# Performance work log

Measured on AMD Instinct MI355X. Metric: run time of the kernel, lower is better.

The kernel has to match this reference:

```python
import jax, jax.numpy as jnp
import numpy as np

EMBED_DIM = 256
NUM_WEIGHTS = 8
NUM_RELATIONS = 5
BATCH = 131072


def setup_inputs() -> dict:
    key = jax.random.key(0)
    k1, k2, k3, k4 = jax.random.split(key, 4)
    embeds1 = jax.random.normal(k1, (BATCH, EMBED_DIM), dtype=jnp.float32)
    embeds2 = jax.random.normal(k2, (BATCH, EMBED_DIM), dtype=jnp.float32)
    # Embedding(num_weights, D*D): torch default init is N(0,1)
    rel_embeds = jax.random.normal(k3, (NUM_WEIGHTS, EMBED_DIM * EMBED_DIM), dtype=jnp.float32)
    # weight_scalars ~ U(-stdv, stdv), stdv = 1/sqrt(num_relations)
    stdv = 1.0 / np.sqrt(NUM_RELATIONS)
    weight_scalars = jax.random.uniform(
        k4, (NUM_WEIGHTS, NUM_RELATIONS), dtype=jnp.float32, minval=-stdv, maxval=stdv
    )
    return {
        "embeds1": embeds1,
        "embeds2": embeds2,
        "rel_embeds": rel_embeds,
        "weight_scalars": weight_scalars,
    }


def reference(embeds1, embeds2, rel_embeds, weight_scalars):
    D = embeds1.shape[1]
    W = rel_embeds.shape[0]
    rel_mats = rel_embeds.reshape(W, D, D)  # [W, D, D]
    # Fused bilinear form u . R_w . v for every w: [B, W]
    basis_outputs = jnp.einsum("bi,wij,bj->bw", embeds1, rel_mats, embeds2)
    logit = basis_outputs @ weight_scalars  # [B, R]
    return logit
```

## Files before the change

kernel.cpp:

```cpp
#include <hip/hip_runtime.h>
#include <hip/hip_bf16.h>

#define ED   256
#define NW   8
#define NR   5
#define BM   64
#define BCOL 128
#define BK   64

typedef float  f32x4  __attribute__((ext_vector_type(4)));
typedef __bf16 bf16x8 __attribute__((ext_vector_type(8)));
typedef unsigned short u16;

__device__ __forceinline__ u16 f2bf(float f) {
    return __builtin_bit_cast(u16, __float2bfloat16(f));
}

__device__ __forceinline__ bf16x8 pack8(f32x4 a, f32x4 b) {
    union { u16 u[8]; bf16x8 v; } r;
    r.u[0] = f2bf(a[0]); r.u[1] = f2bf(a[1]); r.u[2] = f2bf(a[2]); r.u[3] = f2bf(a[3]);
    r.u[4] = f2bf(b[0]); r.u[5] = f2bf(b[1]); r.u[6] = f2bf(b[2]); r.u[7] = f2bf(b[3]);
    return r.v;
}

__global__ void prep_S(const float* __restrict__ rel,
                       const float* __restrict__ ws,
                       u16* __restrict__ S_T) {
    int idx = blockIdx.x * blockDim.x + threadIdx.x;
    if (idx >= ED * ED) return;
    int i = idx & (ED - 1);
    int j = idx >> 8;
    float acc[NR];
#pragma unroll
    for (int r = 0; r < NR; ++r) acc[r] = 0.f;
#pragma unroll
    for (int w = 0; w < NW; ++w) {
        float rv = rel[(size_t)w * ED * ED + (size_t)i * ED + j];
#pragma unroll
        for (int r = 0; r < NR; ++r) acc[r] += rv * ws[w * NR + r];
    }
#pragma unroll
    for (int r = 0; r < NR; ++r)
        S_T[((size_t)r * ED + j) * ED + i] = f2bf(acc[r]);
}

__global__ __launch_bounds__(256, 3) void bilinear_kernel(
    const float* __restrict__ e1, const float* __restrict__ e2,
    const u16* __restrict__ S_T, float* __restrict__ out) {

    __shared__ __align__(16) u16 Bbuf[2][BCOL * BK];
    __shared__ float Red[NR][BM][2];

    const int t    = threadIdx.x;
    const int wave = t >> 6;
    const int lane = t & 63;
    const int l15  = lane & 15;
    const int l4   = lane >> 4;
    const int wr   = wave >> 1;
    const int wc   = wave & 1;

    const int g       = blockIdx.x;
    const int per_xcd = gridDim.x >> 3;
    const int wgid    = (g & 7) * per_xcd + (g >> 3);
    const int ch      = wgid & 1;
    const long b0     = (long)(wgid >> 1) * BM;

    auto STAGE = [&](int rr, int kb, int b) {
        const u16* gb = S_T + ((size_t)rr * ED + ch * BCOL) * ED + kb * BK;
#pragma unroll
        for (int q = 0; q < 4; ++q) {
            int s  = q * 256 + t;
            int j  = s >> 3;
            int c  = s & 7;
            int cl = c ^ (j & 7);
            const u16* gp = gb + (size_t)j * ED + cl * 8;
            u16* lp = &Bbuf[b][(size_t)(q * 256 + wave * 64) * 8];
            __builtin_amdgcn_global_load_lds(
                (const __attribute__((address_space(1))) unsigned int*)gp,
                (__attribute__((address_space(3))) unsigned int*)lp, 16, 0, 0);
        }
    };

    STAGE(0, 0, 0);

    bf16x8 av[2][8];
#pragma unroll
    for (int m = 0; m < 2; ++m) {
        const float* rowp = e1 + (b0 + wr * 32 + m * 16 + l15) * ED + l4 * 8;
#pragma unroll
        for (int kb = 0; kb < 8; ++kb) {
            f32x4 a = *(const f32x4*)(rowp + kb * 32);
            f32x4 b = *(const f32x4*)(rowp + kb * 32 + 4);
            av[m][kb] = pack8(a, b);
        }
    }

    unsigned e2p[2][4][2];
#pragma unroll
    for (int m = 0; m < 2; ++m)
#pragma unroll
        for (int reg = 0; reg < 4; ++reg) {
            const float* erow =
                e2 + (b0 + wr * 32 + m * 16 + l4 * 4 + reg) * ED
                   + ch * BCOL + wc * 64 + l15;
#pragma unroll
            for (int h = 0; h < 2; ++h) {
                float a = __builtin_nontemporal_load(erow + (2 * h) * 16);
                float b = __builtin_nontemporal_load(erow + (2 * h + 1) * 16);
                e2p[m][reg][h] = (unsigned)f2bf(a) | ((unsigned)f2bf(b) << 16);
            }
        }

    __syncthreads();

    for (int r = 0; r < NR; ++r) {
        f32x4 acc[2][4];
#pragma unroll
        for (int m = 0; m < 2; ++m)
#pragma unroll
            for (int n = 0; n < 4; ++n)
                acc[m][n] = f32x4{0.f, 0.f, 0.f, 0.f};

#pragma unroll
        for (int kb = 0; kb < 4; ++kb) {
            const int s   = r * 4 + kb;
            const int cur = s & 1;

            if (s + 1 < NR * 4) {
                const int rn = (kb == 3) ? r + 1 : r;
                const int kn = (kb + 1) & 3;
                STAGE(rn, kn, cur ^ 1);
            }

#pragma unroll
            for (int h = 0; h < 2; ++h) {
                bf16x8 bv[4];
#pragma unroll
                for (int n = 0; n < 4; ++n) {
                    int j  = wc * 64 + n * 16 + l15;
                    int lb = j * (BK * 2) + h * 64 + l4 * 16;
                    int pb = lb ^ ((j & 7) << 4);
                    bv[n] = *(const bf16x8*)((const char*)Bbuf[cur] + pb);
                }
#pragma unroll
                for (int m = 0; m < 2; ++m)
#pragma unroll
                    for (int n = 0; n < 4; ++n)
                        acc[m][n] = __builtin_amdgcn_mfma_f32_16x16x32_bf16(
                            av[m][kb * 2 + h], bv[n], acc[m][n], 0, 0, 0);
            }

            __syncthreads();
        }

#pragma unroll
        for (int m = 0; m < 2; ++m)
#pragma unroll
            for (int reg = 0; reg < 4; ++reg) {
                const int row = wr * 32 + m * 16 + l4 * 4 + reg;
                float p = 0.f;
#pragma unroll
                for (int n = 0; n < 4; ++n) {
                    unsigned u = e2p[m][reg][n >> 1];
                    unsigned bits = (n & 1) ? (u & 0xffff0000u) : (u << 16);
                    p += acc[m][n][reg] * __builtin_bit_cast(float, bits);
                }
#pragma unroll
                for (int off = 1; off < 16; off <<= 1)
                    p += __shfl_xor(p, off);
                if (l15 == 0) Red[r][row][wc] = p;
            }
    }

    __syncthreads();
    for (int idx = t; idx < BM * NR; idx += 256) {
        int row = idx / NR;
        int r   = idx - row * NR;
        atomicAdd(&out[(b0 + row) * NR + r], Red[r][row][0] + Red[r][row][1]);
    }
}

extern "C" void kernel_launch(void* const* d_in, const int* in_sizes, int n_in,
                              void* d_out, int out_size, void* d_ws, size_t ws_size,
                              hipStream_t stream) {
    const float* e1  = (const float*)d_in[0];
    const float* e2  = (const float*)d_in[1];
    const float* rel = (const float*)d_in[2];
    const float* ws  = (const float*)d_in[3];
    float* out = (float*)d_out;
    u16* S_T = (u16*)d_ws;

    prep_S<<<(ED * ED + 255) / 256, 256, 0, stream>>>(rel, ws, S_T);

    hipMemsetAsync(out, 0, (size_t)out_size * sizeof(float), stream);

    int B = in_sizes[0] / ED;
    int grid = (B / BM) * 2;
    bilinear_kernel<<<grid, 256, 0, stream>>>(e1, e2, S_T, out);
}
```

Before: 244.0 us.

## Load S matrix fragments directly from global into registers, drop LDS staging

Replaces the double-buffered LDS staging of the combined relation matrix (global_load_lds plus swizzled LDS reads and per-step barriers) with direct per-lane global loads of bf16x8 fragments into two register buffers. The loads are software-pipelined against the MFMAs, and the relation loop is fully unrolled. This removes the LDS traffic and the __syncthreads between k-steps. In exchange each of the 4 waves now fetches its own B fragments from global/L2, so B data is no longer shared through LDS across the two row-waves, and latency hiding depends on a prefetch distance of one MFMA group.

```diff
diff --git a/kernel.cpp b/kernel.cpp
--- a/kernel.cpp
+++ b/kernel.cpp
@@ -6,7 +6,6 @@
 #define NR   5
 #define BM   64
 #define BCOL 128
-#define BK   64
 
 typedef float  f32x4  __attribute__((ext_vector_type(4)));
 typedef __bf16 bf16x8 __attribute__((ext_vector_type(8)));
@@ -48,7 +47,6 @@
     const float* __restrict__ e1, const float* __restrict__ e2,
     const u16* __restrict__ S_T, float* __restrict__ out) {
 
-    __shared__ __align__(16) u16 Bbuf[2][BCOL * BK];
     __shared__ float Red[NR][BM][2];
 
     const int t    = threadIdx.x;
@@ -65,23 +63,15 @@
     const int ch      = wgid & 1;
     const long b0     = (long)(wgid >> 1) * BM;
 
-    auto STAGE = [&](int rr, int kb, int b) {
-        const u16* gb = S_T + ((size_t)rr * ED + ch * BCOL) * ED + kb * BK;
+    const u16* const Sbase =
+        S_T + ((size_t)(ch * BCOL + wc * 64 + l15)) * ED + l4 * 8;
+
+    bf16x8 bv0[4], bv1[4];
 #pragma unroll
-        for (int q = 0; q < 4; ++q) {
-            int s  = q * 256 + t;
-            int j  = s >> 3;
-            int c  = s & 7;
-            int cl = c ^ (j & 7);
-            const u16* gp = gb + (size_t)j * ED + cl * 8;
-            u16* lp = &Bbuf[b][(size_t)(q * 256 + wave * 64) * 8];
-            __builtin_amdgcn_global_load_lds(
-                (const __attribute__((address_space(1))) unsigned int*)gp,
-                (__attribute__((address_space(3))) unsigned int*)lp, 16, 0, 0);
-        }
-    };
-
-    STAGE(0, 0, 0);
+    for (int n = 0; n < 4; ++n) {
+        bv0[n] = *(const bf16x8*)(Sbase + (size_t)n * 16 * ED);
+        bv1[n] = *(const bf16x8*)(Sbase + (size_t)n * 16 * ED + 32);
+    }
 
     bf16x8 av[2][8];
 #pragma unroll
@@ -111,9 +101,10 @@
             }
         }
 
-    __syncthreads();
+#pragma unroll
+    for (int r = 0; r < NR; ++r) {
+        const u16* const Sr = Sbase + (size_t)r * ED * ED;
 
-    for (int r = 0; r < NR; ++r) {
         f32x4 acc[2][4];
 #pragma unroll
         for (int m = 0; m < 2; ++m)
@@ -122,35 +113,36 @@
                 acc[m][n] = f32x4{0.f, 0.f, 0.f, 0.f};
 
 #pragma unroll
-        for (int kb = 0; kb < 4; ++kb) {
-            const int s   = r * 4 + kb;
-            const int cur = s & 1;
+        for (int kp = 0; kp < 4; ++kp) {
+            const int s = r * 8 + kp * 2;
 
-            if (s + 1 < NR * 4) {
-                const int rn = (kb == 3) ? r + 1 : r;
-                const int kn = (kb + 1) & 3;
-                STAGE(rn, kn, cur ^ 1);
+#pragma unroll
+            for (int m = 0; m < 2; ++m)
+#pragma unroll
+                for (int n = 0; n < 4; ++n)
+                    acc[m][n] = __builtin_amdgcn_mfma_f32_16x16x32_bf16(
+                        av[m][kp * 2], bv0[n], acc[m][n], 0, 0, 0);
+            if (s + 2 < NR * 8) {
+                const u16* p = (kp < 3) ? (Sr + (kp * 2 + 2) * 32)
+                                        : (Sr + ED * ED);
+#pragma unroll
+                for (int n = 0; n < 4; ++n)
+                    bv0[n] = *(const bf16x8*)(p + (size_t)n * 16 * ED);
             }
 
 #pragma unroll
-            for (int h = 0; h < 2; ++h) {
-                bf16x8 bv[4];
+            for (int m = 0; m < 2; ++m)
 #pragma unroll
-                for (int n = 0; n < 4; ++n) {
-                    int j  = wc * 64 + n * 16 + l15;
-                    int lb = j * (BK * 2) + h * 64 + l4 * 16;
-                    int pb = lb ^ ((j & 7) << 4);
-                    bv[n] = *(const bf16x8*)((const char*)Bbuf[cur] + pb);
-                }
+                for (int n = 0; n < 4; ++n)
+                    acc[m][n] = __builtin_amdgcn_mfma_f32_16x16x32_bf16(
+                        av[m][kp * 2 + 1], bv1[n], acc[m][n], 0, 0, 0);
+            if (s + 3 < NR * 8) {
+                const u16* p = (kp < 3) ? (Sr + (kp * 2 + 3) * 32)
+                                        : (Sr + ED * ED + 32);
 #pragma unroll
-                for (int m = 0; m < 2; ++m)
-#pragma unroll
-                    for (int n = 0; n < 4; ++n)
-                        acc[m][n] = __builtin_amdgcn_mfma_f32_16x16x32_bf16(
-                            av[m][kb * 2 + h], bv[n], acc[m][n], 0, 0, 0);
+                for (int n = 0; n < 4; ++n)
+                    bv1[n] = *(const bf16x8*)(p + (size_t)n * 16 * ED);
             }
-
-            __syncthreads();
         }
 
 #pragma unroll
```

After: 439.1 us. 80.0% more time.

## Make S slab LDS-resident and loop persistent workgroups over row passes

Applied to the files above, without the earlier changes.

Each 512-thread workgroup loads a fixed 64-column, 128-k slab of the combined relation matrices for all five relations into LDS once. It then loops over eight passes of 256 batch rows, which removes the per-step double-buffered S staging and its barriers. The grid becomes a fixed 512 blocks split four ways over output columns and two ways over k, so every block reads a different e1/e2 slice and writes partial sums to the output with atomics. The cost is many more global atomics, because there is no LDS reduction before the atomic step. The grid size is hardcoded for the batch of 131072, and there is no prefetch overlap between passes.

```diff
diff --git a/kernel.cpp b/kernel.cpp
--- a/kernel.cpp
+++ b/kernel.cpp
@@ -4,9 +4,10 @@
 #define ED   256
 #define NW   8
 #define NR   5
-#define BM   64
-#define BCOL 128
-#define BK   64
+#define CS   64
+#define KH   128
+#define NPASS 8
+#define RPP  256
 
 typedef float  f32x4  __attribute__((ext_vector_type(4)));
 typedef __bf16 bf16x8 __attribute__((ext_vector_type(8)));
@@ -44,139 +45,120 @@
         S_T[((size_t)r * ED + j) * ED + i] = f2bf(acc[r]);
 }
 
-__global__ __launch_bounds__(256, 3) void bilinear_kernel(
+__global__ __launch_bounds__(512, 4) void bilinear_kernel(
     const float* __restrict__ e1, const float* __restrict__ e2,
     const u16* __restrict__ S_T, float* __restrict__ out) {
 
-    __shared__ __align__(16) u16 Bbuf[2][BCOL * BK];
-    __shared__ float Red[NR][BM][2];
+    __shared__ __align__(16) u16 slab[NR * CS * KH];
 
     const int t    = threadIdx.x;
     const int wave = t >> 6;
     const int lane = t & 63;
     const int l15  = lane & 15;
     const int l4   = lane >> 4;
-    const int wr   = wave >> 1;
-    const int wc   = wave & 1;
 
-    const int g       = blockIdx.x;
-    const int per_xcd = gridDim.x >> 3;
-    const int wgid    = (g & 7) * per_xcd + (g >> 3);
-    const int ch      = wgid & 1;
-    const long b0     = (long)(wgid >> 1) * BM;
+    const int g    = blockIdx.x;
+    const int wgid = (g & 7) * 64 + (g >> 3);
+    const int jc   = wgid & 3;
+    const int kh   = (wgid >> 2) & 1;
+    const int rg   = wgid >> 3;
 
-    auto STAGE = [&](int rr, int kb, int b) {
-        const u16* gb = S_T + ((size_t)rr * ED + ch * BCOL) * ED + kb * BK;
 #pragma unroll
-        for (int q = 0; q < 4; ++q) {
-            int s  = q * 256 + t;
-            int j  = s >> 3;
-            int c  = s & 7;
-            int cl = c ^ (j & 7);
-            const u16* gp = gb + (size_t)j * ED + cl * 8;
-            u16* lp = &Bbuf[b][(size_t)(q * 256 + wave * 64) * 8];
-            __builtin_amdgcn_global_load_lds(
-                (const __attribute__((address_space(1))) unsigned int*)gp,
-                (__attribute__((address_space(3))) unsigned int*)lp, 16, 0, 0);
-        }
-    };
+    for (int q = 0; q < 10; ++q) {
+        int idx = q * 512 + t;
+        int rj  = idx >> 4;
+        int c   = idx & 15;
+        int j   = rj & 63;
+        int r   = rj >> 6;
+        int cl  = c ^ (j & 7);
+        const u16* gp = S_T + ((size_t)(r * ED + jc * CS + j)) * ED
+                            + kh * KH + cl * 8;
+        u16* lp = slab + (size_t)(q * 512 + wave * 64) * 8;
+        __builtin_amdgcn_global_load_lds(
+            (const __attribute__((address_space(1))) unsigned int*)gp,
+            (__attribute__((address_space(3))) unsigned int*)lp, 16, 0, 0);
+    }
+    __syncthreads();
 
-    STAGE(0, 0, 0);
+    for (int pass = 0; pass < NPASS; ++pass) {
+        const long rowbase = (long)rg * (NPASS * RPP) + pass * RPP + wave * 32;
 
-    bf16x8 av[2][8];
+        bf16x8 av[2][4];
 #pragma unroll
-    for (int m = 0; m < 2; ++m) {
-        const float* rowp = e1 + (b0 + wr * 32 + m * 16 + l15) * ED + l4 * 8;
+        for (int m = 0; m < 2; ++m) {
+            const float* rowp =
+                e1 + (rowbase + m * 16 + l15) * ED + kh * KH + l4 * 8;
 #pragma unroll
-        for (int kb = 0; kb < 8; ++kb) {
-            f32x4 a = *(const f32x4*)(rowp + kb * 32);
-            f32x4 b = *(const f32x4*)(rowp + kb * 32 + 4);
-            av[m][kb] = pack8(a, b);
-        }
-    }
-
-    unsigned e2p[2][4][2];
-#pragma unroll
-    for (int m = 0; m < 2; ++m)
-#pragma unroll
-        for (int reg = 0; reg < 4; ++reg) {
-            const float* erow =
-                e2 + (b0 + wr * 32 + m * 16 + l4 * 4 + reg) * ED
-                   + ch * BCOL + wc * 64 + l15;
-#pragma unroll
-            for (int h = 0; h < 2; ++h) {
-                float a = __builtin_nontemporal_load(erow + (2 * h) * 16);
-                float b = __builtin_nontemporal_load(erow + (2 * h + 1) * 16);
-                e2p[m][reg][h] = (unsigned)f2bf(a) | ((unsigned)f2bf(b) << 16);
+            for (int kb = 0; kb < 4; ++kb) {
+                f32x4 a = *(const f32x4*)(rowp + kb * 32);
+                f32x4 b = *(const f32x4*)(rowp + kb * 32 + 4);
+                av[m][kb] = pack8(a, b);
             }
         }
 
-    __syncthreads();
-
-    for (int r = 0; r < NR; ++r) {
-        f32x4 acc[2][4];
+        unsigned e2p[2][4][2];
 #pragma unroll
         for (int m = 0; m < 2; ++m)
 #pragma unroll
-            for (int n = 0; n < 4; ++n)
-                acc[m][n] = f32x4{0.f, 0.f, 0.f, 0.f};
-
+            for (int reg = 0; reg < 4; ++reg) {
+                const float* erow =
+                    e2 + (rowbase + m * 16 + l4 * 4 + reg) * ED + jc * CS + l15;
 #pragma unroll
-        for (int kb = 0; kb < 4; ++kb) {
-            const int s   = r * 4 + kb;
-            const int cur = s & 1;
-
-            if (s + 1 < NR * 4) {
-                const int rn = (kb == 3) ? r + 1 : r;
-                const int kn = (kb + 1) & 3;
-                STAGE(rn, kn, cur ^ 1);
+                for (int h = 0; h < 2; ++h) {
+                    float a = erow[(2 * h) * 16];
+                    float b = erow[(2 * h + 1) * 16];
+                    e2p[m][reg][h] =
+                        (unsigned)f2bf(a) | ((unsigned)f2bf(b) << 16);
+                }
             }
 
 #pragma unroll
-            for (int h = 0; h < 2; ++h) {
+        for (int r = 0; r < NR; ++r) {
+            f32x4 acc[2][4];
+#pragma unroll
+            for (int m = 0; m < 2; ++m)
+#pragma unroll
+                for (int n = 0; n < 4; ++n)
+                    acc[m][n] = f32x4{0.f, 0.f, 0.f, 0.f};
+
+#pragma unroll
+            for (int kb = 0; kb < 4; ++kb) {
                 bf16x8 bv[4];
 #pragma unroll
                 for (int n = 0; n < 4; ++n) {
-                    int j  = wc * 64 + n * 16 + l15;
-                    int lb = j * (BK * 2) + h * 64 + l4 * 16;
-                    int pb = lb ^ ((j & 7) << 4);
-                    bv[n] = *(const bf16x8*)((const char*)Bbuf[cur] + pb);
+                    int j = n * 16 + l15;
+                    int c = (kb * 4 + l4) ^ (j & 7);
+                    bv[n] = *(const bf16x8*)(slab + (size_t)(r * CS + j) * KH
+                                                  + c * 8);
                 }
 #pragma unroll
                 for (int m = 0; m < 2; ++m)
 #pragma unroll
                     for (int n = 0; n < 4; ++n)
                         acc[m][n] = __builtin_amdgcn_mfma_f32_16x16x32_bf16(
-                            av[m][kb * 2 + h], bv[n], acc[m][n], 0, 0, 0);
+                            av[m][kb], bv[n], acc[m][n], 0, 0, 0);
             }
 
-            __syncthreads();
+#pragma unroll
+            for (int m = 0; m < 2; ++m)
+#pragma unroll
+                for (int reg = 0; reg < 4; ++reg) {
+                    float p = 0.f;
+#pragma unroll
+                    for (int n = 0; n < 4; ++n) {
+                        unsigned u = e2p[m][reg][n >> 1];
+                        unsigned bits = (n & 1) ? (u & 0xffff0000u) : (u << 16);
+                        p += acc[m][n][reg] * __builtin_bit_cast(float, bits);
+                    }
+#pragma unroll
+                    for (int off = 1; off < 16; off <<= 1)
+                        p += __shfl_xor(p, off);
+                    if (l15 == 0) {
+                        long row = rowbase + m * 16 + l4 * 4 + reg;
+                        atomicAdd(&out[row * NR + r], p);
+                    }
+                }
         }
-
-#pragma unroll
-        for (int m = 0; m < 2; ++m)
-#pragma unroll
-            for (int reg = 0; reg < 4; ++reg) {
-                const int row = wr * 32 + m * 16 + l4 * 4 + reg;
-                float p = 0.f;
-#pragma unroll
-                for (int n = 0; n < 4; ++n) {
-                    unsigned u = e2p[m][reg][n >> 1];
-                    unsigned bits = (n & 1) ? (u & 0xffff0000u) : (u << 16);
-                    p += acc[m][n][reg] * __builtin_bit_cast(float, bits);
-                }
-#pragma unroll
-                for (int off = 1; off < 16; off <<= 1)
-                    p += __shfl_xor(p, off);
-                if (l15 == 0) Red[r][row][wc] = p;
-            }
-    }
-
-    __syncthreads();
-    for (int idx = t; idx < BM * NR; idx += 256) {
-        int row = idx / NR;
-        int r   = idx - row * NR;
-        atomicAdd(&out[(b0 + row) * NR + r], Red[r][row][0] + Red[r][row][1]);
     }
 }
 
@@ -194,7 +176,5 @@
 
     hipMemsetAsync(out, 0, (size_t)out_size * sizeof(float), stream);
 
-    int B = in_sizes[0] / ED;
-    int grid = (B / BM) * 2;
-    bilinear_kernel<<<grid, 256, 0, stream>>>(e1, e2, S_T, out);
+    bilinear_kernel<<<512, 512, 0, stream>>>(e1, e2, S_T, out);
 }
```

After: 697.8 us. +186.0%, slower.
